# Kernel tuning notes

Measured on AMD Instinct MI355X. Metric: run time of the kernel, lower is better.

Reference implementation:

```python
import jax, jax.numpy as jnp
import numpy as np

N = 100000
E = 1280000
D = 64


def setup_inputs() -> dict:
    key = jax.random.key(0)
    k1, k2, k3, k4, k5, k6 = jax.random.split(key, 6)
    return {
        "x": jax.random.normal(k1, (N, D), dtype=jnp.float32),
        "w_src": jax.random.normal(k2, (D,), dtype=jnp.float32),
        "w_dst": jax.random.normal(k3, (D,), dtype=jnp.float32),
        "ew": jax.random.normal(k4, (E,), dtype=jnp.float32),
        "src_idx": jax.random.randint(k5, (E,), 0, N, dtype=jnp.int64),
        "dst_idx": jax.random.randint(k6, (E,), 0, N, dtype=jnp.int64),
    }


def reference(x, w_src, w_dst, ew, src_idx, dst_idx):
    # Per-node scalar scores: Linear(emb_dim, 1, bias=False)
    a_src = x @ w_src            # [N]
    a_dst = x @ w_dst            # [N]
    # Edge attention: tanh(a_src[u] + a_dst[v]) * ew  (u_add_v + tanh + scale)
    a = jnp.tanh(a_src[src_idx] + a_dst[dst_idx]) * ew   # [E]
    # Message = a_e * x[src_e]; reduce = scatter-sum over dst (u_mul_e + sum)
    m = a[:, None] * x[src_idx]                           # [E, D]
    h = jax.ops.segment_sum(m, dst_idx, num_segments=N)   # [N, D]
    return h
```

## Files before the change

kernel.cpp:

```cpp
#include <hip/hip_runtime.h>
#include <hip/hip_fp16.h>
#include <math.h>

#define DIM  64
#define SPAN 256
#define NBIN 256
#define KMAX 512
#define CAP  6144

__global__ void score_kernel(const float* __restrict__ x,
                             const float* __restrict__ w_src,
                             const float* __restrict__ w_dst,
                             float* __restrict__ a_src,
                             float* __restrict__ a_dst,
                             int N) {
    int gid  = blockIdx.x * blockDim.x + threadIdx.x;
    int node = gid >> 6;
    int lane = threadIdx.x & 63;
    if (node >= N) return;
    float xv = x[(size_t)node * DIM + lane];
    float s1 = xv * w_src[lane];
    float s2 = xv * w_dst[lane];
    #pragma unroll
    for (int off = 32; off > 0; off >>= 1) {
        s1 += __shfl_down(s1, off, 64);
        s2 += __shfl_down(s2, off, 64);
    }
    if (lane == 0) {
        a_src[node] = s1;
        a_dst[node] = s2;
    }
}

__global__ void xhalf_kernel(const float* __restrict__ x,
                             __half* __restrict__ xh, int total2) {
    int i = blockIdx.x * blockDim.x + threadIdx.x;
    if (i >= total2) return;
    float2 v = ((const float2*)x)[i];
    ((__half2*)xh)[i] = __floats2half2_rn(v.x, v.y);
}

__global__ __launch_bounds__(1024) void hist_coarse(
        const int* __restrict__ dst, int* __restrict__ cnt,
        int E, int N, int K) {
    __shared__ int lh[KMAX];
    int tid = threadIdx.x;
    for (int j = tid; j < K; j += blockDim.x) lh[j] = 0;
    __syncthreads();
    for (int base = blockIdx.x * 1024; base < E; base += NBIN * 1024) {
        int e = base + tid;
        if (e < E) {
            unsigned t = (unsigned)dst[e];
            if (t >= (unsigned)N) t = 0;
            atomicAdd(&lh[t >> 8], 1);
        }
    }
    __syncthreads();
    for (int j = tid; j < K; j += blockDim.x)
        cnt[j * NBIN + blockIdx.x] = lh[j];
}

__global__ void scan_part(const int* __restrict__ cnt, int* __restrict__ offs,
                          int* __restrict__ bsum, int N) {
    __shared__ int buf[2][256];
    int tid = threadIdx.x;
    int i = blockIdx.x * 256 + tid;
    int v = (i < N) ? cnt[i] : 0;
    int sel = 0;
    buf[0][tid] = v;
    __syncthreads();
    for (int off = 1; off < 256; off <<= 1) {
        int nsel = sel ^ 1;
        buf[nsel][tid] = buf[sel][tid] + ((tid >= off) ? buf[sel][tid - off] : 0);
        __syncthreads();
        sel = nsel;
    }
    if (i < N) offs[i] = buf[sel][tid] - v;
    if (tid == 255) bsum[blockIdx.x] = buf[sel][255];
}

__global__ void scan_top(int* __restrict__ bsum, int* __restrict__ offs,
                         int NB, int N) {
    __shared__ int buf[2][512];
    int tid = threadIdx.x;
    int v = (tid < NB) ? bsum[tid] : 0;
    int sel = 0;
    buf[0][tid] = v;
    __syncthreads();
    for (int off = 1; off < 512; off <<= 1) {
        int nsel = sel ^ 1;
        buf[nsel][tid] = buf[sel][tid] + ((tid >= off) ? buf[sel][tid - off] : 0);
        __syncthreads();
        sel = nsel;
    }
    if (tid < NB) bsum[tid] = buf[sel][tid] - v;
    if (tid == 511) offs[N] = buf[sel][511];
}

__global__ __launch_bounds__(1024) void binpass_kernel(
        const float* __restrict__ ew,
        const int* __restrict__ src_idx,
        const int* __restrict__ dst_idx,
        const float* __restrict__ a_src,
        const float* __restrict__ a_dst,
        const int* __restrict__ moffs,
        const int* __restrict__ bsum,
        unsigned long long* __restrict__ pay,
        int E, int N, int K) {
    __shared__ int lcur[KMAX];
    int tid = threadIdx.x;
    for (int j = tid; j < K; j += blockDim.x) {
        int i = j * NBIN + blockIdx.x;
        lcur[j] = moffs[i] + bsum[i >> 8];
    }
    __syncthreads();
    for (int base = blockIdx.x * 1024; base < E; base += NBIN * 1024) {
        int e = base + tid;
        if (e < E) {
            unsigned s = (unsigned)src_idx[e];
            unsigned t = (unsigned)dst_idx[e];
            if (s >= (unsigned)N) s = 0;
            if (t >= (unsigned)N) t = 0;
            float a = tanhf(a_src[s] + a_dst[t]) * ew[e];
            int bk = (int)(t >> 8);
            int pos = atomicAdd(&lcur[bk], 1);
            unsigned rec = (s << 8) | (t & 255u);
            pay[pos] = ((unsigned long long)rec << 32) |
                       (unsigned long long)__float_as_uint(a);
        }
    }
}

__global__ __launch_bounds__(1024) void bucket_sort_kernel(
        const float* __restrict__ x,
        unsigned long long* __restrict__ pay,
        const int* __restrict__ moffs,
        const int* __restrict__ bsum,
        int* __restrict__ startv,
        int* __restrict__ endv,
        float* __restrict__ h,
        int N, int K, int E) {
    __shared__ unsigned long long srec[CAP];
    __shared__ int hcnt[SPAN];
    __shared__ int hoff[2][SPAN];
    __shared__ int lcur[SPAN];
    int tid = threadIdx.x;
    int b   = blockIdx.x;
    int i0 = b * NBIN;
    int bstart = moffs[i0] + bsum[i0 >> 8];
    int bend;
    if (b == K - 1) bend = E;
    else { int i1 = (b + 1) * NBIN; bend = moffs[i1] + bsum[i1 >> 8]; }
    int cnt = bend - bstart;

    if (cnt <= CAP) {
        if (tid < SPAN) hcnt[tid] = 0;
        __syncthreads();
        for (int i = tid; i < cnt; i += 1024) {
            unsigned long long r = pay[bstart + i];
            srec[i] = r;
            atomicAdd(&hcnt[(int)((r >> 32) & 255u)], 1);
        }
        __syncthreads();
        int sel = 0;
        if (tid < SPAN) hoff[0][tid] = hcnt[tid];
        __syncthreads();
        for (int off = 1; off < SPAN; off <<= 1) {
            int nsel = sel ^ 1;
            if (tid < SPAN)
                hoff[nsel][tid] = hoff[sel][tid] +
                                  ((tid >= off) ? hoff[sel][tid - off] : 0);
            __syncthreads();
            sel = nsel;
        }
        if (tid < SPAN) {
            int incl = hoff[sel][tid];
            int excl = incl - hcnt[tid];
            lcur[tid] = bstart + excl;
            int node = b * SPAN + tid;
            if (node < N) {
                startv[node] = bstart + excl;
                endv[node]   = bstart + incl;
            }
        }
        __syncthreads();
        for (int i = tid; i < cnt; i += 1024) {
            unsigned long long r = srec[i];
            int d = (int)((r >> 32) & 255u);
            int pos = atomicAdd(&lcur[d], 1);
            pay[pos] = r;
        }
    } else {
        if (tid < SPAN) {
            int node = b * SPAN + tid;
            if (node < N) startv[node] = -1;
        }
        for (int j = tid; j < SPAN * DIM; j += 1024) {
            int node = b * SPAN + (j >> 6);
            if (node < N) h[(size_t)node * DIM + (j & 63)] = 0.f;
        }
        __syncthreads();
        for (int i = tid; i < cnt; i += 1024) {
            unsigned long long r = pay[bstart + i];
            unsigned s = (unsigned)(r >> 40);
            if (s >= (unsigned)N) s = 0;
            int node = b * SPAN + (int)((r >> 32) & 255u);
            float a = __uint_as_float((unsigned)r);
            if (node < N)
                for (int k = 0; k < DIM; ++k)
                    atomicAdd(&h[(size_t)node * DIM + k],
                              a * x[(size_t)s * DIM + k]);
        }
    }
}

__global__ void gather_f16_kernel(const __half* __restrict__ xh,
                                  const unsigned long long* __restrict__ pay,
                                  const int* __restrict__ startv,
                                  const int* __restrict__ endv,
                                  float* __restrict__ h,
                                  int N, int E) {
    int gid  = blockIdx.x * blockDim.x + threadIdx.x;
    int t    = gid >> 6;
    int lane = threadIdx.x & 63;
    if (t >= N) return;
    int p = startv[t];
    if (p < 0) return;
    int end = endv[t];
    if (end > E) end = E;
    float a0 = 0.f, a1 = 0.f, a2 = 0.f, a3 = 0.f;

    while (p + 8 <= end) {
        unsigned long long r0 = pay[p];
        unsigned long long r1 = pay[p + 1];
        unsigned long long r2 = pay[p + 2];
        unsigned long long r3 = pay[p + 3];
        unsigned long long r4 = pay[p + 4];
        unsigned long long r5 = pay[p + 5];
        unsigned long long r6 = pay[p + 6];
        unsigned long long r7 = pay[p + 7];
        p += 8;
        unsigned s0 = (unsigned)(r0 >> 40); if (s0 >= (unsigned)N) s0 = 0;
        unsigned s1 = (unsigned)(r1 >> 40); if (s1 >= (unsigned)N) s1 = 0;
        unsigned s2 = (unsigned)(r2 >> 40); if (s2 >= (unsigned)N) s2 = 0;
        unsigned s3 = (unsigned)(r3 >> 40); if (s3 >= (unsigned)N) s3 = 0;
        unsigned s4 = (unsigned)(r4 >> 40); if (s4 >= (unsigned)N) s4 = 0;
        unsigned s5 = (unsigned)(r5 >> 40); if (s5 >= (unsigned)N) s5 = 0;
        unsigned s6 = (unsigned)(r6 >> 40); if (s6 >= (unsigned)N) s6 = 0;
        unsigned s7 = (unsigned)(r7 >> 40); if (s7 >= (unsigned)N) s7 = 0;
        float x0 = __half2float(xh[(size_t)s0 * DIM + lane]);
        float x1 = __half2float(xh[(size_t)s1 * DIM + lane]);
        float x2 = __half2float(xh[(size_t)s2 * DIM + lane]);
        float x3 = __half2float(xh[(size_t)s3 * DIM + lane]);
        float x4 = __half2float(xh[(size_t)s4 * DIM + lane]);
        float x5 = __half2float(xh[(size_t)s5 * DIM + lane]);
        float x6 = __half2float(xh[(size_t)s6 * DIM + lane]);
        float x7 = __half2float(xh[(size_t)s7 * DIM + lane]);
        a0 = fmaf(__uint_as_float((unsigned)r0), x0, a0);
        a1 = fmaf(__uint_as_float((unsigned)r1), x1, a1);
        a2 = fmaf(__uint_as_float((unsigned)r2), x2, a2);
        a3 = fmaf(__uint_as_float((unsigned)r3), x3, a3);
        a0 = fmaf(__uint_as_float((unsigned)r4), x4, a0);
        a1 = fmaf(__uint_as_float((unsigned)r5), x5, a1);
        a2 = fmaf(__uint_as_float((unsigned)r6), x6, a2);
        a3 = fmaf(__uint_as_float((unsigned)r7), x7, a3);
    }
    if (p + 4 <= end) {
        unsigned long long r0 = pay[p];
        unsigned long long r1 = pay[p + 1];
        unsigned long long r2 = pay[p + 2];
        unsigned long long r3 = pay[p + 3];
        p += 4;
        unsigned s0 = (unsigned)(r0 >> 40); if (s0 >= (unsigned)N) s0 = 0;
        unsigned s1 = (unsigned)(r1 >> 40); if (s1 >= (unsigned)N) s1 = 0;
        unsigned s2 = (unsigned)(r2 >> 40); if (s2 >= (unsigned)N) s2 = 0;
        unsigned s3 = (unsigned)(r3 >> 40); if (s3 >= (unsigned)N) s3 = 0;
        float x0 = __half2float(xh[(size_t)s0 * DIM + lane]);
        float x1 = __half2float(xh[(size_t)s1 * DIM + lane]);
        float x2 = __half2float(xh[(size_t)s2 * DIM + lane]);
        float x3 = __half2float(xh[(size_t)s3 * DIM + lane]);
        a0 = fmaf(__uint_as_float((unsigned)r0), x0, a0);
        a1 = fmaf(__uint_as_float((unsigned)r1), x1, a1);
        a2 = fmaf(__uint_as_float((unsigned)r2), x2, a2);
        a3 = fmaf(__uint_as_float((unsigned)r3), x3, a3);
    }
    if (p + 2 <= end) {
        unsigned long long r0 = pay[p];
        unsigned long long r1 = pay[p + 1];
        p += 2;
        unsigned s0 = (unsigned)(r0 >> 40); if (s0 >= (unsigned)N) s0 = 0;
        unsigned s1 = (unsigned)(r1 >> 40); if (s1 >= (unsigned)N) s1 = 0;
        a0 = fmaf(__uint_as_float((unsigned)r0),
                  __half2float(xh[(size_t)s0 * DIM + lane]), a0);
        a1 = fmaf(__uint_as_float((unsigned)r1),
                  __half2float(xh[(size_t)s1 * DIM + lane]), a1);
    }
    if (p < end) {
        unsigned long long r0 = pay[p];
        unsigned s0 = (unsigned)(r0 >> 40); if (s0 >= (unsigned)N) s0 = 0;
        a0 = fmaf(__uint_as_float((unsigned)r0),
                  __half2float(xh[(size_t)s0 * DIM + lane]), a0);
    }
    h[(size_t)t * DIM + lane] = (a0 + a1) + (a2 + a3);
}

__global__ void gather_f32_kernel(const float* __restrict__ x,
                                  const unsigned long long* __restrict__ pay,
                                  const int* __restrict__ startv,
                                  const int* __restrict__ endv,
                                  float* __restrict__ h,
                                  int N, int E) {
    int gid  = blockIdx.x * blockDim.x + threadIdx.x;
    int t    = gid >> 6;
    int lane = threadIdx.x & 63;
    if (t >= N) return;
    int p = startv[t];
    if (p < 0) return;
    int end = endv[t];
    if (end > E) end = E;
    float a0 = 0.f, a1 = 0.f, a2 = 0.f, a3 = 0.f;
    while (p + 4 <= end) {
        unsigned long long r0 = pay[p];
        unsigned long long r1 = pay[p + 1];
        unsigned long long r2 = pay[p + 2];
        unsigned long long r3 = pay[p + 3];
        p += 4;
        unsigned s0 = (unsigned)(r0 >> 40); if (s0 >= (unsigned)N) s0 = 0;
        unsigned s1 = (unsigned)(r1 >> 40); if (s1 >= (unsigned)N) s1 = 0;
        unsigned s2 = (unsigned)(r2 >> 40); if (s2 >= (unsigned)N) s2 = 0;
        unsigned s3 = (unsigned)(r3 >> 40); if (s3 >= (unsigned)N) s3 = 0;
        a0 = fmaf(__uint_as_float((unsigned)r0), x[(size_t)s0 * DIM + lane], a0);
        a1 = fmaf(__uint_as_float((unsigned)r1), x[(size_t)s1 * DIM + lane], a1);
        a2 = fmaf(__uint_as_float((unsigned)r2), x[(size_t)s2 * DIM + lane], a2);
        a3 = fmaf(__uint_as_float((unsigned)r3), x[(size_t)s3 * DIM + lane], a3);
    }
    for (; p < end; ++p) {
        unsigned long long r0 = pay[p];
        unsigned s0 = (unsigned)(r0 >> 40); if (s0 >= (unsigned)N) s0 = 0;
        a0 = fmaf(__uint_as_float((unsigned)r0), x[(size_t)s0 * DIM + lane], a0);
    }
    h[(size_t)t * DIM + lane] = (a0 + a1) + (a2 + a3);
}

__global__ void zero_h_kernel(float* __restrict__ p, int n) {
    int i = blockIdx.x * blockDim.x + threadIdx.x;
    if (i < n) p[i] = 0.f;
}

__global__ void edge_kernel_atomic(const float* __restrict__ x,
                                   const float* __restrict__ ew,
                                   const int* __restrict__ src_idx,
                                   const int* __restrict__ dst_idx,
                                   const float* __restrict__ a_src,
                                   const float* __restrict__ a_dst,
                                   float* __restrict__ h,
                                   int E) {
    int gid  = blockIdx.x * blockDim.x + threadIdx.x;
    int e    = gid >> 6;
    int lane = threadIdx.x & 63;
    if (e >= E) return;
    int s = src_idx[e];
    int t = dst_idx[e];
    float a  = tanhf(a_src[s] + a_dst[t]) * ew[e];
    float xv = x[(size_t)s * DIM + lane];
    atomicAdd(&h[(size_t)t * DIM + lane], a * xv);
}

extern "C" void kernel_launch(void* const* d_in, const int* in_sizes, int n_in,
                              void* d_out, int out_size, void* d_ws, size_t ws_size,
                              hipStream_t stream) {
    const float* x     = (const float*)d_in[0];
    const float* w_src = (const float*)d_in[1];
    const float* w_dst = (const float*)d_in[2];
    const float* ew    = (const float*)d_in[3];
    const int*   src   = (const int*)d_in[4];
    const int*   dst   = (const int*)d_in[5];
    float* h = (float*)d_out;

    int N = in_sizes[0] / DIM;
    int E = in_sizes[3];

    int K    = (N + SPAN - 1) / SPAN;
    int Ntot = K * NBIN;
    int NBs  = (Ntot + 255) / 256;

    float* a_src  = (float*)d_ws;
    float* a_dst  = a_src + N;
    int*   startv = (int*)(a_dst + N);
    int*   endv   = startv + N;
    int*   moffs  = endv + N;
    int*   bsum   = moffs + Ntot + 1;
    size_t head_bytes = ((size_t)(4 * N) + (size_t)Ntot + 1 + (size_t)NBs) * 4;
    size_t pay_off = (head_bytes + 15) & ~(size_t)15;
    unsigned long long* pay = (unsigned long long*)((char*)d_ws + pay_off);
    size_t xh_off = pay_off + (size_t)E * 8;
    __half* xh = (__half*)((char*)d_ws + xh_off);
    size_t need_sort = pay_off + (size_t)E * 8;
    size_t need_f16  = xh_off + (size_t)N * DIM * 2;

    int score_blocks = (N + 3) / 4;
    score_kernel<<<score_blocks, 256, 0, stream>>>(x, w_src, w_dst, a_src, a_dst, N);

    if (ws_size < need_sort || K > KMAX || NBs > 512) {
        int ob = (out_size + 255) / 256;
        zero_h_kernel<<<ob, 256, 0, stream>>>(h, out_size);
        int edge_blocks = (E + 3) / 4;
        edge_kernel_atomic<<<edge_blocks, 256, 0, stream>>>(x, ew, src, dst,
                                                            a_src, a_dst, h, E);
        return;
    }

    bool use_f16 = (ws_size >= need_f16);
    if (use_f16) {
        int total2 = N * DIM / 2;
        xhalf_kernel<<<(total2 + 255) / 256, 256, 0, stream>>>(x, xh, total2);
    }

    hist_coarse<<<NBIN, 1024, 0, stream>>>(dst, moffs, E, N, K);
    scan_part<<<NBs, 256, 0, stream>>>(moffs, moffs, bsum, Ntot);
    scan_top<<<1, 512, 0, stream>>>(bsum, moffs, NBs, Ntot);
    binpass_kernel<<<NBIN, 1024, 0, stream>>>(ew, src, dst, a_src, a_dst,
                                              moffs, bsum, pay, E, N, K);
    bucket_sort_kernel<<<K, 1024, 0, stream>>>(x, pay, moffs, bsum,
                                               startv, endv, h, N, K, E);
    int gather_blocks = (N + 3) / 4;
    if (use_f16)
        gather_f16_kernel<<<gather_blocks, 256, 0, stream>>>(xh, pay, startv,
                                                             endv, h, N, E);
    else
        gather_f32_kernel<<<gather_blocks, 256, 0, stream>>>(x, pay, startv,
                                                             endv, h, N, E);
}
```

Before: 196.8 us.

## Fuse bucket sort with gather and fold fp16 conversion into score kernel

The per-bucket sort now keeps records in shared memory and builds a local index array, then each wave accumulates one destination node's messages straight from LDS. This removes the write-back of the sorted payload, the start/end arrays and the separate gather kernel launch. The fp16 copy of x is written by the score kernel, which drops a separate conversion pass over x. In exchange the fused kernel runs only K (~391) blocks of 1024 threads with larger shared memory use, so the gather phase may have less parallelism and occupancy than the old N-wave gather launch.

```diff
diff --git a/kernel.cpp b/kernel.cpp
--- a/kernel.cpp
+++ b/kernel.cpp
@@ -13,12 +13,14 @@
                              const float* __restrict__ w_dst,
                              float* __restrict__ a_src,
                              float* __restrict__ a_dst,
+                             __half* __restrict__ xh,
                              int N) {
     int gid  = blockIdx.x * blockDim.x + threadIdx.x;
     int node = gid >> 6;
     int lane = threadIdx.x & 63;
     if (node >= N) return;
     float xv = x[(size_t)node * DIM + lane];
+    xh[(size_t)node * DIM + lane] = __float2half_rn(xv);
     float s1 = xv * w_src[lane];
     float s2 = xv * w_dst[lane];
     #pragma unroll
@@ -30,14 +32,6 @@
         a_src[node] = s1;
         a_dst[node] = s2;
     }
-}
-
-__global__ void xhalf_kernel(const float* __restrict__ x,
-                             __half* __restrict__ xh, int total2) {
-    int i = blockIdx.x * blockDim.x + threadIdx.x;
-    if (i >= total2) return;
-    float2 v = ((const float2*)x)[i];
-    ((__half2*)xh)[i] = __floats2half2_rn(v.x, v.y);
 }
 
 __global__ __launch_bounds__(1024) void hist_coarse(
@@ -131,19 +125,20 @@
     }
 }
 
-__global__ __launch_bounds__(1024) void bucket_sort_kernel(
-        const float* __restrict__ x,
-        unsigned long long* __restrict__ pay,
+__global__ __launch_bounds__(1024) void sort_gather_kernel(
+        const __half* __restrict__ xh,
+        const float* __restrict__ x32,
+        const unsigned long long* __restrict__ pay,
         const int* __restrict__ moffs,
         const int* __restrict__ bsum,
-        int* __restrict__ startv,
-        int* __restrict__ endv,
         float* __restrict__ h,
         int N, int K, int E) {
     __shared__ unsigned long long srec[CAP];
+    __shared__ unsigned short sidx[CAP];
     __shared__ int hcnt[SPAN];
     __shared__ int hoff[2][SPAN];
     __shared__ int lcur[SPAN];
+    __shared__ int nstart[SPAN];
     int tid = threadIdx.x;
     int b   = blockIdx.x;
     int i0 = b * NBIN;
@@ -174,27 +169,100 @@
             sel = nsel;
         }
         if (tid < SPAN) {
-            int incl = hoff[sel][tid];
-            int excl = incl - hcnt[tid];
-            lcur[tid] = bstart + excl;
-            int node = b * SPAN + tid;
-            if (node < N) {
-                startv[node] = bstart + excl;
-                endv[node]   = bstart + incl;
-            }
+            int excl = hoff[sel][tid] - hcnt[tid];
+            nstart[tid] = excl;
+            lcur[tid]   = excl;
         }
         __syncthreads();
         for (int i = tid; i < cnt; i += 1024) {
             unsigned long long r = srec[i];
             int d = (int)((r >> 32) & 255u);
             int pos = atomicAdd(&lcur[d], 1);
-            pay[pos] = r;
+            sidx[pos] = (unsigned short)i;
+        }
+        __syncthreads();
+        int lane = tid & 63;
+        int wave = tid >> 6;
+        for (int d = wave; d < SPAN; d += 16) {
+            int node = b * SPAN + d;
+            if (node >= N) break;
+            int p  = nstart[d];
+            int pe = p + hcnt[d];
+            float a0 = 0.f, a1 = 0.f, a2 = 0.f, a3 = 0.f;
+            while (p + 8 <= pe) {
+                unsigned long long r0 = srec[sidx[p]];
+                unsigned long long r1 = srec[sidx[p + 1]];
+                unsigned long long r2 = srec[sidx[p + 2]];
+                unsigned long long r3 = srec[sidx[p + 3]];
+                unsigned long long r4 = srec[sidx[p + 4]];
+                unsigned long long r5 = srec[sidx[p + 5]];
+                unsigned long long r6 = srec[sidx[p + 6]];
+                unsigned long long r7 = srec[sidx[p + 7]];
+                p += 8;
+                unsigned s0 = (unsigned)(r0 >> 40); if (s0 >= (unsigned)N) s0 = 0;
+                unsigned s1 = (unsigned)(r1 >> 40); if (s1 >= (unsigned)N) s1 = 0;
+                unsigned s2 = (unsigned)(r2 >> 40); if (s2 >= (unsigned)N) s2 = 0;
+                unsigned s3 = (unsigned)(r3 >> 40); if (s3 >= (unsigned)N) s3 = 0;
+                unsigned s4 = (unsigned)(r4 >> 40); if (s4 >= (unsigned)N) s4 = 0;
+                unsigned s5 = (unsigned)(r5 >> 40); if (s5 >= (unsigned)N) s5 = 0;
+                unsigned s6 = (unsigned)(r6 >> 40); if (s6 >= (unsigned)N) s6 = 0;
+                unsigned s7 = (unsigned)(r7 >> 40); if (s7 >= (unsigned)N) s7 = 0;
+                float x0 = __half2float(xh[(size_t)s0 * DIM + lane]);
+                float x1 = __half2float(xh[(size_t)s1 * DIM + lane]);
+                float x2 = __half2float(xh[(size_t)s2 * DIM + lane]);
+                float x3 = __half2float(xh[(size_t)s3 * DIM + lane]);
+                float x4 = __half2float(xh[(size_t)s4 * DIM + lane]);
+                float x5 = __half2float(xh[(size_t)s5 * DIM + lane]);
+                float x6 = __half2float(xh[(size_t)s6 * DIM + lane]);
+                float x7 = __half2float(xh[(size_t)s7 * DIM + lane]);
+                a0 = fmaf(__uint_as_float((unsigned)r0), x0, a0);
+                a1 = fmaf(__uint_as_float((unsigned)r1), x1, a1);
+                a2 = fmaf(__uint_as_float((unsigned)r2), x2, a2);
+                a3 = fmaf(__uint_as_float((unsigned)r3), x3, a3);
+                a0 = fmaf(__uint_as_float((unsigned)r4), x4, a0);
+                a1 = fmaf(__uint_as_float((unsigned)r5), x5, a1);
+                a2 = fmaf(__uint_as_float((unsigned)r6), x6, a2);
+                a3 = fmaf(__uint_as_float((unsigned)r7), x7, a3);
+            }
+            if (p + 4 <= pe) {
+                unsigned long long r0 = srec[sidx[p]];
+                unsigned long long r1 = srec[sidx[p + 1]];
+                unsigned long long r2 = srec[sidx[p + 2]];
+                unsigned long long r3 = srec[sidx[p + 3]];
+                p += 4;
+                unsigned s0 = (unsigned)(r0 >> 40); if (s0 >= (unsigned)N) s0 = 0;
+                unsigned s1 = (unsigned)(r1 >> 40); if (s1 >= (unsigned)N) s1 = 0;
+                unsigned s2 = (unsigned)(r2 >> 40); if (s2 >= (unsigned)N) s2 = 0;
+                unsigned s3 = (unsigned)(r3 >> 40); if (s3 >= (unsigned)N) s3 = 0;
+                float x0 = __half2float(xh[(size_t)s0 * DIM + lane]);
+                float x1 = __half2float(xh[(size_t)s1 * DIM + lane]);
+                float x2 = __half2float(xh[(size_t)s2 * DIM + lane]);
+                float x3 = __half2float(xh[(size_t)s3 * DIM + lane]);
+                a0 = fmaf(__uint_as_float((unsigned)r0), x0, a0);
+                a1 = fmaf(__uint_as_float((unsigned)r1), x1, a1);
+                a2 = fmaf(__uint_as_float((unsigned)r2), x2, a2);
+                a3 = fmaf(__uint_as_float((unsigned)r3), x3, a3);
+            }
+            if (p + 2 <= pe) {
+                unsigned long long r0 = srec[sidx[p]];
+                unsigned long long r1 = srec[sidx[p + 1]];
+                p += 2;
+                unsigned s0 = (unsigned)(r0 >> 40); if (s0 >= (unsigned)N) s0 = 0;
+                unsigned s1 = (unsigned)(r1 >> 40); if (s1 >= (unsigned)N) s1 = 0;
+                a0 = fmaf(__uint_as_float((unsigned)r0),
+                          __half2float(xh[(size_t)s0 * DIM + lane]), a0);
+                a1 = fmaf(__uint_as_float((unsigned)r1),
+                          __half2float(xh[(size_t)s1 * DIM + lane]), a1);
+            }
+            if (p < pe) {
+                unsigned long long r0 = srec[sidx[p]];
+                unsigned s0 = (unsigned)(r0 >> 40); if (s0 >= (unsigned)N) s0 = 0;
+                a0 = fmaf(__uint_as_float((unsigned)r0),
+                          __half2float(xh[(size_t)s0 * DIM + lane]), a0);
+            }
+            h[(size_t)node * DIM + lane] = (a0 + a1) + (a2 + a3);
         }
     } else {
-        if (tid < SPAN) {
-            int node = b * SPAN + tid;
-            if (node < N) startv[node] = -1;
-        }
         for (int j = tid; j < SPAN * DIM; j += 1024) {
             int node = b * SPAN + (j >> 6);
             if (node < N) h[(size_t)node * DIM + (j & 63)] = 0.f;
@@ -209,137 +277,9 @@
             if (node < N)
                 for (int k = 0; k < DIM; ++k)
                     atomicAdd(&h[(size_t)node * DIM + k],
-                              a * x[(size_t)s * DIM + k]);
-        }
-    }
-}
-
-__global__ void gather_f16_kernel(const __half* __restrict__ xh,
-                                  const unsigned long long* __restrict__ pay,
-                                  const int* __restrict__ startv,
-                                  const int* __restrict__ endv,
-                                  float* __restrict__ h,
-                                  int N, int E) {
-    int gid  = blockIdx.x * blockDim.x + threadIdx.x;
-    int t    = gid >> 6;
-    int lane = threadIdx.x & 63;
-    if (t >= N) return;
-    int p = startv[t];
-    if (p < 0) return;
-    int end = endv[t];
-    if (end > E) end = E;
-    float a0 = 0.f, a1 = 0.f, a2 = 0.f, a3 = 0.f;
-
-    while (p + 8 <= end) {
-        unsigned long long r0 = pay[p];
-        unsigned long long r1 = pay[p + 1];
-        unsigned long long r2 = pay[p + 2];
-        unsigned long long r3 = pay[p + 3];
-        unsigned long long r4 = pay[p + 4];
-        unsigned long long r5 = pay[p + 5];
-        unsigned long long r6 = pay[p + 6];
-        unsigned long long r7 = pay[p + 7];
-        p += 8;
-        unsigned s0 = (unsigned)(r0 >> 40); if (s0 >= (unsigned)N) s0 = 0;
-        unsigned s1 = (unsigned)(r1 >> 40); if (s1 >= (unsigned)N) s1 = 0;
-        unsigned s2 = (unsigned)(r2 >> 40); if (s2 >= (unsigned)N) s2 = 0;
-        unsigned s3 = (unsigned)(r3 >> 40); if (s3 >= (unsigned)N) s3 = 0;
-        unsigned s4 = (unsigned)(r4 >> 40); if (s4 >= (unsigned)N) s4 = 0;
-        unsigned s5 = (unsigned)(r5 >> 40); if (s5 >= (unsigned)N) s5 = 0;
-        unsigned s6 = (unsigned)(r6 >> 40); if (s6 >= (unsigned)N) s6 = 0;
-        unsigned s7 = (unsigned)(r7 >> 40); if (s7 >= (unsigned)N) s7 = 0;
-        float x0 = __half2float(xh[(size_t)s0 * DIM + lane]);
-        float x1 = __half2float(xh[(size_t)s1 * DIM + lane]);
-        float x2 = __half2float(xh[(size_t)s2 * DIM + lane]);
-        float x3 = __half2float(xh[(size_t)s3 * DIM + lane]);
-        float x4 = __half2float(xh[(size_t)s4 * DIM + lane]);
-        float x5 = __half2float(xh[(size_t)s5 * DIM + lane]);
-        float x6 = __half2float(xh[(size_t)s6 * DIM + lane]);
-        float x7 = __half2float(xh[(size_t)s7 * DIM + lane]);
-        a0 = fmaf(__uint_as_float((unsigned)r0), x0, a0);
-        a1 = fmaf(__uint_as_float((unsigned)r1), x1, a1);
-        a2 = fmaf(__uint_as_float((unsigned)r2), x2, a2);
-        a3 = fmaf(__uint_as_float((unsigned)r3), x3, a3);
-        a0 = fmaf(__uint_as_float((unsigned)r4), x4, a0);
-        a1 = fmaf(__uint_as_float((unsigned)r5), x5, a1);
-        a2 = fmaf(__uint_as_float((unsigned)r6), x6, a2);
-        a3 = fmaf(__uint_as_float((unsigned)r7), x7, a3);
-    }
-    if (p + 4 <= end) {
-        unsigned long long r0 = pay[p];
-        unsigned long long r1 = pay[p + 1];
-        unsigned long long r2 = pay[p + 2];
-        unsigned long long r3 = pay[p + 3];
-        p += 4;
-        unsigned s0 = (unsigned)(r0 >> 40); if (s0 >= (unsigned)N) s0 = 0;
-        unsigned s1 = (unsigned)(r1 >> 40); if (s1 >= (unsigned)N) s1 = 0;
-        unsigned s2 = (unsigned)(r2 >> 40); if (s2 >= (unsigned)N) s2 = 0;
-        unsigned s3 = (unsigned)(r3 >> 40); if (s3 >= (unsigned)N) s3 = 0;
-        float x0 = __half2float(xh[(size_t)s0 * DIM + lane]);
-        float x1 = __half2float(xh[(size_t)s1 * DIM + lane]);
-        float x2 = __half2float(xh[(size_t)s2 * DIM + lane]);
-        float x3 = __half2float(xh[(size_t)s3 * DIM + lane]);
-        a0 = fmaf(__uint_as_float((unsigned)r0), x0, a0);
-        a1 = fmaf(__uint_as_float((unsigned)r1), x1, a1);
-        a2 = fmaf(__uint_as_float((unsigned)r2), x2, a2);
-        a3 = fmaf(__uint_as_float((unsigned)r3), x3, a3);
-    }
-    if (p + 2 <= end) {
-        unsigned long long r0 = pay[p];
-        unsigned long long r1 = pay[p + 1];
-        p += 2;
-        unsigned s0 = (unsigned)(r0 >> 40); if (s0 >= (unsigned)N) s0 = 0;
-        unsigned s1 = (unsigned)(r1 >> 40); if (s1 >= (unsigned)N) s1 = 0;
-        a0 = fmaf(__uint_as_float((unsigned)r0),
-                  __half2float(xh[(size_t)s0 * DIM + lane]), a0);
-        a1 = fmaf(__uint_as_float((unsigned)r1),
-                  __half2float(xh[(size_t)s1 * DIM + lane]), a1);
-    }
-    if (p < end) {
-        unsigned long long r0 = pay[p];
-        unsigned s0 = (unsigned)(r0 >> 40); if (s0 >= (unsigned)N) s0 = 0;
-        a0 = fmaf(__uint_as_float((unsigned)r0),
-                  __half2float(xh[(size_t)s0 * DIM + lane]), a0);
-    }
-    h[(size_t)t * DIM + lane] = (a0 + a1) + (a2 + a3);
-}
-
-__global__ void gather_f32_kernel(const float* __restrict__ x,
-                                  const unsigned long long* __restrict__ pay,
-                                  const int* __restrict__ startv,
-                                  const int* __restrict__ endv,
-                                  float* __restrict__ h,
-                                  int N, int E) {
-    int gid  = blockIdx.x * blockDim.x + threadIdx.x;
-    int t    = gid >> 6;
-    int lane = threadIdx.x & 63;
-    if (t >= N) return;
-    int p = startv[t];
-    if (p < 0) return;
-    int end = endv[t];
-    if (end > E) end = E;
-    float a0 = 0.f, a1 = 0.f, a2 = 0.f, a3 = 0.f;
-    while (p + 4 <= end) {
-        unsigned long long r0 = pay[p];
-        unsigned long long r1 = pay[p + 1];
-        unsigned long long r2 = pay[p + 2];
-        unsigned long long r3 = pay[p + 3];
-        p += 4;
-        unsigned s0 = (unsigned)(r0 >> 40); if (s0 >= (unsigned)N) s0 = 0;
-        unsigned s1 = (unsigned)(r1 >> 40); if (s1 >= (unsigned)N) s1 = 0;
-        unsigned s2 = (unsigned)(r2 >> 40); if (s2 >= (unsigned)N) s2 = 0;
-        unsigned s3 = (unsigned)(r3 >> 40); if (s3 >= (unsigned)N) s3 = 0;
-        a0 = fmaf(__uint_as_float((unsigned)r0), x[(size_t)s0 * DIM + lane], a0);
-        a1 = fmaf(__uint_as_float((unsigned)r1), x[(size_t)s1 * DIM + lane], a1);
-        a2 = fmaf(__uint_as_float((unsigned)r2), x[(size_t)s2 * DIM + lane], a2);
-        a3 = fmaf(__uint_as_float((unsigned)r3), x[(size_t)s3 * DIM + lane], a3);
-    }
-    for (; p < end; ++p) {
-        unsigned long long r0 = pay[p];
-        unsigned s0 = (unsigned)(r0 >> 40); if (s0 >= (unsigned)N) s0 = 0;
-        a0 = fmaf(__uint_as_float((unsigned)r0), x[(size_t)s0 * DIM + lane], a0);
-    }
-    h[(size_t)t * DIM + lane] = (a0 + a1) + (a2 + a3);
+                              a * x32[(size_t)s * DIM + k]);
+        }
+    }
 }
 
 __global__ void zero_h_kernel(float* __restrict__ p, int n) {
@@ -366,6 +306,30 @@
     atomicAdd(&h[(size_t)t * DIM + lane], a * xv);
 }
 
+__global__ void score_only_kernel(const float* __restrict__ x,
+                                  const float* __restrict__ w_src,
+                                  const float* __restrict__ w_dst,
+                                  float* __restrict__ a_src,
+                                  float* __restrict__ a_dst,
+                                  int N) {
+    int gid  = blockIdx.x * blockDim.x + threadIdx.x;
+    int node = gid >> 6;
+    int lane = threadIdx.x & 63;
+    if (node >= N) return;
+    float xv = x[(size_t)node * DIM + lane];
+    float s1 = xv * w_src[lane];
+    float s2 = xv * w_dst[lane];
+    #pragma unroll
+    for (int off = 32; off > 0; off >>= 1) {
+        s1 += __shfl_down(s1, off, 64);
+        s2 += __shfl_down(s2, off, 64);
+    }
+    if (lane == 0) {
+        a_src[node] = s1;
+        a_dst[node] = s2;
+    }
+}
+
 extern "C" void kernel_launch(void* const* d_in, const int* in_sizes, int n_in,
                               void* d_out, int out_size, void* d_ws, size_t ws_size,
                               hipStream_t stream) {
@@ -386,22 +350,20 @@
 
     float* a_src  = (float*)d_ws;
     float* a_dst  = a_src + N;
-    int*   startv = (int*)(a_dst + N);
-    int*   endv   = startv + N;
-    int*   moffs  = endv + N;
+    int*   moffs  = (int*)(a_dst + N);
     int*   bsum   = moffs + Ntot + 1;
-    size_t head_bytes = ((size_t)(4 * N) + (size_t)Ntot + 1 + (size_t)NBs) * 4;
+    size_t head_bytes = ((size_t)(2 * N) + (size_t)Ntot + 1 + (size_t)NBs) * 4;
     size_t pay_off = (head_bytes + 15) & ~(size_t)15;
     unsigned long long* pay = (unsigned long long*)((char*)d_ws + pay_off);
     size_t xh_off = pay_off + (size_t)E * 8;
     __half* xh = (__half*)((char*)d_ws + xh_off);
-    size_t need_sort = pay_off + (size_t)E * 8;
-    size_t need_f16  = xh_off + (size_t)N * DIM * 2;
+    size_t need = xh_off + (size_t)N * DIM * 2;
 
     int score_blocks = (N + 3) / 4;
-    score_kernel<<<score_blocks, 256, 0, stream>>>(x, w_src, w_dst, a_src, a_dst, N);
-
-    if (ws_size < need_sort || K > KMAX || NBs > 512) {
+
+    if (ws_size < need || K > KMAX || NBs > 512 || (N * DIM) % 2 != 0) {
+        score_only_kernel<<<score_blocks, 256, 0, stream>>>(x, w_src, w_dst,
+                                                            a_src, a_dst, N);
         int ob = (out_size + 255) / 256;
         zero_h_kernel<<<ob, 256, 0, stream>>>(h, out_size);
         int edge_blocks = (E + 3) / 4;
@@ -410,24 +372,13 @@
         return;
     }
 
-    bool use_f16 = (ws_size >= need_f16);
-    if (use_f16) {
-        int total2 = N * DIM / 2;
-        xhalf_kernel<<<(total2 + 255) / 256, 256, 0, stream>>>(x, xh, total2);
-    }
-
+    score_kernel<<<score_blocks, 256, 0, stream>>>(x, w_src, w_dst,
+                                                   a_src, a_dst, xh, N);
     hist_coarse<<<NBIN, 1024, 0, stream>>>(dst, moffs, E, N, K);
     scan_part<<<NBs, 256, 0, stream>>>(moffs, moffs, bsum, Ntot);
     scan_top<<<1, 512, 0, stream>>>(bsum, moffs, NBs, Ntot);
     binpass_kernel<<<NBIN, 1024, 0, stream>>>(ew, src, dst, a_src, a_dst,
                                               moffs, bsum, pay, E, N, K);
-    bucket_sort_kernel<<<K, 1024, 0, stream>>>(x, pay, moffs, bsum,
-                                               startv, endv, h, N, K, E);
-    int gather_blocks = (N + 3) / 4;
-    if (use_f16)
-        gather_f16_kernel<<<gather_blocks, 256, 0, stream>>>(xh, pay, startv,
-                                                             endv, h, N, E);
-    else
-        gather_f32_kernel<<<gather_blocks, 256, 0, stream>>>(x, pay, startv,
-                                                             endv, h, N, E);
-}
+    sort_gather_kernel<<<K, 1024, 0, stream>>>(xh, x, pay, moffs, bsum,
+                                               h, N, K, E);
+}
```

Result: faster. 185.9 us (-5.5%).
